# Optimization experiments

Hardware: AMD Instinct MI355X
Metric: run time of the kernel (lower is better)

Reference implementation:

```python
import jax, jax.numpy as jnp
import numpy as np

B, S, H = 8, 1024, 1024
NH, HD = 16, 64
MBANK, TOPK = 128, 16
NLAYERS, FF = 12, 4096
EPS = 1e-5


def _ln(x, w, b):
    m = x.mean(-1, keepdims=True)
    v = ((x - m) ** 2).mean(-1, keepdims=True)
    return (x - m) / jnp.sqrt(v + EPS) * w + b


def _split_heads(x):  # [B,S,H] -> [B,NH,S,HD]
    return x.reshape(B, S, NH, HD).transpose(0, 2, 1, 3)


def _sdpa(q, k, v):  # inputs [B,NH,S,HD]
    scores = jnp.einsum('bhqd,bhkd->bhqk', q, k) / jnp.sqrt(jnp.float32(HD))
    attn = jax.nn.softmax(scores, axis=-1)
    o = jnp.einsum('bhqk,bhkd->bhqd', attn, v)
    return o.transpose(0, 2, 1, 3).reshape(B, S, H)


def setup_inputs() -> dict:
    key = jax.random.key(0)
    ks = jax.random.split(key, 24)
    n = lambda k, shp, s=0.02: jax.random.normal(k, shp, jnp.float32) * s
    return {
        'hidden_states': jax.random.normal(ks[0], (B, S, H), jnp.float32),
        'ln1_w': jnp.ones((H,), jnp.float32), 'ln1_b': jnp.zeros((H,), jnp.float32),
        'ln2_w': jnp.ones((H,), jnp.float32), 'ln2_b': jnp.zeros((H,), jnp.float32),
        'rec_wq': n(ks[1], (H, H)), 'rec_wk': n(ks[2], (H, H)),
        'rec_wv': n(ks[3], (H, H)), 'rec_wo': n(ks[4], (H, H)),
        'rec_ad_w1': n(ks[5], (H // 4, H)), 'rec_ad_w2': n(ks[6], (H, H // 4)),
        'mem_bank': n(ks[7], (MBANK, H)),
        'alloc_w': n(ks[8], (MBANK, H)), 'alloc_b': jnp.zeros((MBANK,), jnp.float32),
        'retr_w': n(ks[9], (MBANK, H)), 'retr_b': jnp.zeros((MBANK,), jnp.float32),
        'upd_w': n(ks[10], (H, H)), 'upd_b': jnp.zeros((H,), jnp.float32),
        'mem_scales': jnp.full((NLAYERS,), 0.1, jnp.float32),
        'attn_in_w': n(ks[11], (3 * H, H)), 'attn_in_b': jnp.zeros((3 * H,), jnp.float32),
        'attn_out_w': n(ks[12], (H, H)), 'attn_out_b': jnp.zeros((H,), jnp.float32),
        'mlp_w1': n(ks[13], (FF, H)), 'mlp_b1': jnp.zeros((FF,), jnp.float32),
        'mlp_w2': n(ks[14], (H, FF)), 'mlp_b2': jnp.zeros((H,), jnp.float32),
        'layer_idx': 4,
    }


def reference(hidden_states, ln1_w, ln1_b, ln2_w, ln2_b,
              rec_wq, rec_wk, rec_wv, rec_wo, rec_ad_w1, rec_ad_w2,
              mem_bank, alloc_w, alloc_b, retr_w, retr_b, upd_w, upd_b, mem_scales,
              attn_in_w, attn_in_b, attn_out_w, attn_out_b,
              mlp_w1, mlp_b1, mlp_w2, mlp_b2, layer_idx):
    residual = hidden_states
    h = _ln(hidden_states, ln1_w, ln1_b)

    # --- CrossLayerParameterRecycler (layer_idx % 4 == 0 and > 0 -> recycle) ---
    if layer_idx % 4 == 0 and layer_idx > 0:
        q = _split_heads(h @ rec_wq.T)
        k = _split_heads(h @ rec_wk.T)
        v = _split_heads(h @ rec_wv.T)
        base_out = _sdpa(q, k, v) @ rec_wo.T
        h = jax.nn.relu(base_out @ rec_ad_w1.T) @ rec_ad_w2.T

    # --- CrossLayerMemoryManager ---
    pooled = h.mean(axis=1)                                  # [B,H]
    alloc_weights = jax.nn.softmax(pooled @ alloc_w.T + alloc_b, axis=-1)   # [B,MBANK]
    retr_weights = jax.nn.softmax(pooled @ retr_w.T + retr_b, axis=-1)
    retrieved = retr_weights @ mem_bank                      # [B,H]
    h = h + retrieved[:, None, :] * mem_scales[layer_idx]
    update_signals = jax.nn.sigmoid(h.mean(axis=1) @ upd_w.T + upd_b)       # [B,H]
    _, top_idx = jax.lax.top_k(alloc_weights, TOPK)          # [B,TOPK]

    # sequential per-batch scatter (later batches overwrite earlier, as in torch loop)
    def _write(mb, be):
        idx, sig = be
        return mb.at[idx].set(jnp.broadcast_to(sig, (TOPK, H))), None
    new_mem_bank, _ = jax.lax.scan(_write, mem_bank, (top_idx, update_signals))

    # --- self attention (nn.MultiheadAttention, batch_first) ---
    qkv = h @ attn_in_w.T + attn_in_b                        # [B,S,3H]
    q, k, v = jnp.split(qkv, 3, axis=-1)
    attn_out = _sdpa(_split_heads(q), _split_heads(k), _split_heads(v))
    attn_out = attn_out @ attn_out_w.T + attn_out_b
    h = residual + attn_out

    # --- MLP block ---
    residual2 = h
    h = _ln(h, ln2_w, ln2_b)
    h = jax.nn.gelu(h @ mlp_w1.T + mlp_b1, approximate=False) @ mlp_w2.T + mlp_b2
    out = residual2 + h
    return out, new_mem_bank
```

## Files before the change

### kernel.cpp

```cpp
#include <hip/hip_runtime.h>
#include <hip/hip_bf16.h>
#include <math.h>
#include <stdint.h>


#define BB 8
#define SS 1024
#define HH 1024
#define NHEAD 16
#define HD 64
#define MBANK 128
#define TOPK_N 16
#define FF_DIM 4096
#define MROWS (BB * SS)
#define NB_ELEM (8ull*1024*1024)

typedef __bf16 bf16x8 __attribute__((ext_vector_type(8)));
typedef __bf16 bf16x4 __attribute__((ext_vector_type(4)));
typedef float f32x4 __attribute__((ext_vector_type(4)));

#define SCALE_LOG2E 0.18033688011112042f

__device__ __forceinline__ unsigned short f2b(float x) {
  unsigned u = __float_as_uint(x);
  unsigned r = (u + 0x7FFFu + ((u >> 16) & 1u)) >> 16;
  return (unsigned short)r;
}
__device__ __forceinline__ float b2f(unsigned short u) {
  return __uint_as_float((unsigned)u << 16);
}

__device__ __forceinline__ float hmax4(f32x4 v) {
  return fmaxf(fmaxf(v[0], v[1]), fmaxf(v[2], v[3]));
}

__device__ __forceinline__ void load16_lds(const void* g, void* lds_base, int lane) {
#if __has_builtin(__builtin_amdgcn_global_load_lds)
  typedef const __attribute__((address_space(1))) unsigned int guint;
  typedef __attribute__((address_space(3))) unsigned int luint;
  __builtin_amdgcn_global_load_lds((guint*)(uintptr_t)g,
                                   (luint*)(unsigned long long)(unsigned int)(uintptr_t)lds_base,
                                   16, 0, 0);
#else
  *(uint4*)((char*)lds_base + lane * 16) = *(const uint4*)g;
#endif
}

__device__ __forceinline__ float gelu_exact(float x) {
  return 0.5f * x * (1.f + erff(x * 0.70710678118654752440f));
}


__global__ __launch_bounds__(256) void cast_split(const float* __restrict__ s,
                                                  unsigned short* __restrict__ hi,
                                                  unsigned short* __restrict__ lo, int n4) {
  int i = blockIdx.x * 256 + threadIdx.x;
  if (i < n4) {
    float4 v = ((const float4*)s)[i];
    ushort4 h, l;
    h.x = f2b(v.x); l.x = f2b(v.x - b2f(h.x));
    h.y = f2b(v.y); l.y = f2b(v.y - b2f(h.y));
    h.z = f2b(v.z); l.z = f2b(v.z - b2f(h.z));
    h.w = f2b(v.w); l.w = f2b(v.w - b2f(h.w));
    ((ushort4*)hi)[i] = h;
    ((ushort4*)lo)[i] = l;
  }
}

__global__ __launch_bounds__(256) void ln3(const float* __restrict__ x,
                                           const float* __restrict__ w,
                                           const float* __restrict__ b,
                                           unsigned short* __restrict__ yh,
                                           unsigned short* __restrict__ yl) {
  int row = blockIdx.x;
  const float* xr = x + (size_t)row * HH;
  int t = threadIdx.x;
  float v[4];
  float s = 0.f, ss = 0.f;
#pragma unroll
  for (int i = 0; i < 4; i++) {
    v[i] = xr[t + i * 256];
    s += v[i];
    ss += v[i] * v[i];
  }
  __shared__ float rs[8], rss[8];
  for (int o = 32; o > 0; o >>= 1) {
    s += __shfl_down(s, o, 64);
    ss += __shfl_down(ss, o, 64);
  }
  int wid = t >> 6, lane = t & 63;
  if (lane == 0) { rs[wid] = s; rss[wid] = ss; }
  __syncthreads();
  if (t == 0) {
    float S = rs[0] + rs[1] + rs[2] + rs[3];
    float SSum = rss[0] + rss[1] + rss[2] + rss[3];
    float m = S * (1.f / HH);
    float var = SSum * (1.f / HH) - m * m;
    rs[4] = m;
    rs[5] = rsqrtf(var + 1e-5f);
  }
  __syncthreads();
  float m = rs[4], inv = rs[5];
#pragma unroll
  for (int i = 0; i < 4; i++) {
    int c = t + i * 256;
    float y = (v[i] - m) * inv * w[c] + b[c];
    unsigned short h = f2b(y);
    yh[(size_t)row * HH + c] = h;
    yl[(size_t)row * HH + c] = f2b(y - b2f(h));
  }
}

template <int ACT, int MODE>
__global__ __launch_bounds__(256) void gemm3(const unsigned short* __restrict__ Ah,
                                             const unsigned short* __restrict__ Al, int lda,
                                             const unsigned short* __restrict__ Wh,
                                             const unsigned short* __restrict__ Wl, int ldw,
                                             unsigned short* __restrict__ Oh,
                                             unsigned short* __restrict__ Ol,
                                             float* __restrict__ outF,
                                             int ldo, int K) {
  __shared__ unsigned short Ash[128 * 32];
  __shared__ unsigned short Asl[128 * 32];
  __shared__ unsigned short Bsh[128 * 32];
  __shared__ unsigned short Bsl[128 * 32];
  int n0 = blockIdx.x * 128, m0 = blockIdx.y * 128;
  int t = threadIdx.x, w = t >> 6, L = t & 63, quad = L >> 4, l16 = L & 15;
  int wm = w & 1, wn = w >> 1;
  const f32x4 vzero = {0.f, 0.f, 0.f, 0.f};
  f32x4 acc[4][4];
#pragma unroll
  for (int i = 0; i < 4; i++)
#pragma unroll
    for (int j = 0; j < 4; j++) acc[i][j] = vzero;
  int srow = L >> 2;
  int scol = ((L & 3) ^ ((L >> 3) & 3)) * 8;
  int rsw = (l16 >> 1) & 3;
  for (int k0 = 0; k0 < K; k0 += 32) {
    __syncthreads();
#pragma unroll
    for (int c = 0; c < 2; c++) {
      int r = (c * 4 + w) * 16 + srow;
      size_t aoff = (size_t)(m0 + r) * lda + k0 + scol;
      size_t boff = (size_t)(n0 + r) * ldw + k0 + scol;
      load16_lds(Ah + aoff, &Ash[(c * 4 + w) * 512], L);
      load16_lds(Al + aoff, &Asl[(c * 4 + w) * 512], L);
      load16_lds(Wh + boff, &Bsh[(c * 4 + w) * 512], L);
      load16_lds(Wl + boff, &Bsl[(c * 4 + w) * 512], L);
    }
    __syncthreads();
    bf16x8 afh[4], afl[4], bfh[4], bfl[4];
#pragma unroll
    for (int i = 0; i < 4; i++) {
      int off = (wm * 64 + i * 16 + l16) * 32 + (quad ^ rsw) * 8;
      afh[i] = *(const bf16x8*)&Ash[off];
      afl[i] = *(const bf16x8*)&Asl[off];
    }
#pragma unroll
    for (int j = 0; j < 4; j++) {
      int off = (wn * 64 + j * 16 + l16) * 32 + (quad ^ rsw) * 8;
      bfh[j] = *(const bf16x8*)&Bsh[off];
      bfl[j] = *(const bf16x8*)&Bsl[off];
    }
#pragma unroll
    for (int i = 0; i < 4; i++)
#pragma unroll
      for (int j = 0; j < 4; j++) {
        acc[i][j] = __builtin_amdgcn_mfma_f32_16x16x32_bf16(afh[i], bfh[j], acc[i][j], 0, 0, 0);
        acc[i][j] = __builtin_amdgcn_mfma_f32_16x16x32_bf16(afh[i], bfl[j], acc[i][j], 0, 0, 0);
        acc[i][j] = __builtin_amdgcn_mfma_f32_16x16x32_bf16(afl[i], bfh[j], acc[i][j], 0, 0, 0);
      }
  }
#pragma unroll
  for (int i = 0; i < 4; i++) {
    int mb = m0 + wm * 64 + i * 16 + quad * 4;
#pragma unroll
    for (int j = 0; j < 4; j++) {
      int n = n0 + wn * 64 + j * 16 + l16;
      if (MODE == 1) {
        ushort4 sh, sl;
        float vv[4];
#pragma unroll
        for (int r = 0; r < 4; r++) {
          float v = acc[i][j][r];
          if (ACT == 1) v = fmaxf(v, 0.f);
          vv[r] = v;
        }
        sh.x = f2b(vv[0]); sl.x = f2b(vv[0] - b2f(sh.x));
        sh.y = f2b(vv[1]); sl.y = f2b(vv[1] - b2f(sh.y));
        sh.z = f2b(vv[2]); sl.z = f2b(vv[2] - b2f(sh.z));
        sh.w = f2b(vv[3]); sl.w = f2b(vv[3] - b2f(sh.w));
        *(ushort4*)&Oh[(size_t)n * ldo + mb] = sh;
        *(ushort4*)&Ol[(size_t)n * ldo + mb] = sl;
      } else {
#pragma unroll
        for (int r = 0; r < 4; r++) {
          float v = acc[i][j][r];
          if (ACT == 1) v = fmaxf(v, 0.f);
          size_t off = (size_t)(mb + r) * ldo + n;
          if (MODE == 0) {
            unsigned short h = f2b(v);
            Oh[off] = h;
            Ol[off] = f2b(v - b2f(h));
          } else {
            outF[off] = v;
          }
        }
      }
    }
  }
}

__global__ __launch_bounds__(256) void sdpa3(const unsigned short* __restrict__ Qh,
                                             const unsigned short* __restrict__ Ql,
                                             const unsigned short* __restrict__ Kh,
                                             const unsigned short* __restrict__ Kl,
                                             const unsigned short* __restrict__ Vth,
                                             const unsigned short* __restrict__ Vtl,
                                             unsigned short* __restrict__ Oh,
                                             unsigned short* __restrict__ Ol) {
  __shared__ unsigned short Ksh[64 * 64];
  __shared__ unsigned short Ksl[64 * 64];
  __shared__ unsigned short Vsh[64 * 64];
  __shared__ unsigned short Vsl[64 * 64];
  __shared__ __align__(16) unsigned short Psh[4][16 * 64];
  __shared__ __align__(16) unsigned short Psl[4][16 * 64];
  int qt = blockIdx.x, h = blockIdx.y, b = blockIdx.z;
  int t = threadIdx.x, w = t >> 6, L = t & 63, quad = L >> 4, l16 = L & 15;
  int q0 = qt * 64;
  const f32x4 vzero = {0.f, 0.f, 0.f, 0.f};
  bf16x8 qfh[2], qfl[2];
  {
    size_t qrow = (size_t)(b * SS + q0 + w * 16 + l16);
#pragma unroll
    for (int kh = 0; kh < 2; kh++) {
      size_t off = qrow * HH + h * 64 + kh * 32 + quad * 8;
      qfh[kh] = *(const bf16x8*)&Qh[off];
      qfl[kh] = *(const bf16x8*)&Ql[off];
    }
  }
  float mprev = -1e30f, lsum = 0.f;
  f32x4 oacc[4];
#pragma unroll
  for (int jd = 0; jd < 4; jd++) oacc[jd] = vzero;
  int srow = L >> 3, scol = ((L & 7) ^ (L >> 3)) * 8;
  int k7 = l16 & 7;
  unsigned short* Pwh = &Psh[w][0];
  unsigned short* Pwl = &Psl[w][0];
  for (int k0 = 0; k0 < SS; k0 += 64) {
    __syncthreads();
#pragma unroll
    for (int c = 0; c < 2; c++) {
      int rr = (c * 4 + w) * 8 + srow;
      size_t koff = (size_t)(b * SS + k0 + rr) * HH + h * 64 + scol;
      size_t voff = (size_t)(h * 64 + rr) * MROWS + b * SS + k0 + scol;
      load16_lds(Kh + koff, &Ksh[(c * 4 + w) * 512], L);
      load16_lds(Kl + koff, &Ksl[(c * 4 + w) * 512], L);
      load16_lds(Vth + voff, &Vsh[(c * 4 + w) * 512], L);
      load16_lds(Vtl + voff, &Vsl[(c * 4 + w) * 512], L);
    }
    __syncthreads();
    f32x4 sacc[4];
#pragma unroll
    for (int jn = 0; jn < 4; jn++) sacc[jn] = vzero;
#pragma unroll
    for (int jn = 0; jn < 4; jn++)
#pragma unroll
      for (int kh = 0; kh < 2; kh++) {
        int off = (jn * 16 + l16) * 64 + ((kh * 4 + quad) ^ k7) * 8;
        bf16x8 kfh = *(const bf16x8*)&Ksh[off];
        bf16x8 kfl = *(const bf16x8*)&Ksl[off];
        sacc[jn] = __builtin_amdgcn_mfma_f32_16x16x32_bf16(kfh, qfh[kh], sacc[jn], 0, 0, 0);
        sacc[jn] = __builtin_amdgcn_mfma_f32_16x16x32_bf16(kfl, qfh[kh], sacc[jn], 0, 0, 0);
        sacc[jn] = __builtin_amdgcn_mfma_f32_16x16x32_bf16(kfh, qfl[kh], sacc[jn], 0, 0, 0);
      }
    float mt = fmaxf(fmaxf(hmax4(sacc[0]), hmax4(sacc[1])),
                     fmaxf(hmax4(sacc[2]), hmax4(sacc[3])));
    mt = fmaxf(mt, __shfl_xor(mt, 16, 64));
    mt = fmaxf(mt, __shfl_xor(mt, 32, 64));
    float m2 = fmaxf(mprev, mt * SCALE_LOG2E);
    float alpha = exp2f(mprev - m2);
    mprev = m2;
    float rs = 0.f;
#pragma unroll
    for (int jn = 0; jn < 4; jn++) {
      float p0 = exp2f(fmaf(sacc[jn][0], SCALE_LOG2E, -m2));
      float p1 = exp2f(fmaf(sacc[jn][1], SCALE_LOG2E, -m2));
      float p2 = exp2f(fmaf(sacc[jn][2], SCALE_LOG2E, -m2));
      float p3 = exp2f(fmaf(sacc[jn][3], SCALE_LOG2E, -m2));
      rs += (p0 + p1) + (p2 + p3);
      bf16x4 ph, pl;
      ph[0] = (__bf16)p0; pl[0] = (__bf16)(p0 - (float)ph[0]);
      ph[1] = (__bf16)p1; pl[1] = (__bf16)(p1 - (float)ph[1]);
      ph[2] = (__bf16)p2; pl[2] = (__bf16)(p2 - (float)ph[2]);
      ph[3] = (__bf16)p3; pl[3] = (__bf16)(p3 - (float)ph[3]);
      int pidx = l16 * 64 + (((jn * 2 + (quad >> 1)) ^ k7) << 3) + ((quad & 1) << 2);
      *(bf16x4*)&Pwh[pidx] = ph;
      *(bf16x4*)&Pwl[pidx] = pl;
    }
    rs += __shfl_xor(rs, 16, 64);
    rs += __shfl_xor(rs, 32, 64);
    lsum = lsum * alpha + rs;
    float ar[4];
#pragma unroll
    for (int r = 0; r < 4; r++) ar[r] = __shfl(alpha, quad * 4 + r, 16);
#pragma unroll
    for (int jd = 0; jd < 4; jd++)
#pragma unroll
      for (int r = 0; r < 4; r++) oacc[jd][r] *= ar[r];
    bf16x8 pfh[2], pfl[2];
#pragma unroll
    for (int kh = 0; kh < 2; kh++) {
      int off = l16 * 64 + (((kh * 4 + quad) ^ k7) << 3);
      pfh[kh] = *(const bf16x8*)&Pwh[off];
      pfl[kh] = *(const bf16x8*)&Pwl[off];
    }
#pragma unroll
    for (int jd = 0; jd < 4; jd++)
#pragma unroll
      for (int kh = 0; kh < 2; kh++) {
        int off = (jd * 16 + l16) * 64 + ((kh * 4 + quad) ^ k7) * 8;
        bf16x8 vfh = *(const bf16x8*)&Vsh[off];
        bf16x8 vfl = *(const bf16x8*)&Vsl[off];
        oacc[jd] = __builtin_amdgcn_mfma_f32_16x16x32_bf16(pfh[kh], vfh, oacc[jd], 0, 0, 0);
        oacc[jd] = __builtin_amdgcn_mfma_f32_16x16x32_bf16(pfh[kh], vfl, oacc[jd], 0, 0, 0);
        oacc[jd] = __builtin_amdgcn_mfma_f32_16x16x32_bf16(pfl[kh], vfh, oacc[jd], 0, 0, 0);
      }
  }
  float inv = 1.f / lsum;
  float invr[4];
#pragma unroll
  for (int r = 0; r < 4; r++) invr[r] = __shfl(inv, quad * 4 + r, 16);
#pragma unroll
  for (int r = 0; r < 4; r++) {
    size_t row = (size_t)(b * SS + q0 + w * 16 + quad * 4 + r);
#pragma unroll
    for (int jd = 0; jd < 4; jd++) {
      float v = oacc[jd][r] * invr[r];
      unsigned short hh = f2b(v);
      size_t off = row * HH + h * 64 + jd * 16 + l16;
      Oh[off] = hh;
      Ol[off] = f2b(v - b2f(hh));
    }
  }
}


__global__ __launch_bounds__(256) void meanpool_kernel(const float* __restrict__ Hb,
                                                       float* __restrict__ P) {
  int cb = blockIdx.x;
  int b = blockIdx.y;
  int t = threadIdx.x;
  int c = (t & 63) + cb * 64;
  int part = t >> 6;
  float s = 0.f;
  const float* p = Hb + ((size_t)b * SS + part * 256) * HH + c;
  for (int j = 0; j < 256; j++) s += p[(size_t)j * HH];
  __shared__ float red[4][64];
  red[part][t & 63] = s;
  __syncthreads();
  if (t < 64) {
    float tot = red[0][t] + red[1][t] + red[2][t] + red[3][t];
    P[b * HH + cb * 64 + t] = tot * (1.f / SS);
  }
}

__global__ __launch_bounds__(256) void memlogits_kernel(const float* __restrict__ P,
                                                        const float* __restrict__ AW,
                                                        const float* __restrict__ ABias,
                                                        const float* __restrict__ RW,
                                                        const float* __restrict__ RBias,
                                                        float* __restrict__ LA,
                                                        float* __restrict__ LR) {
  int m = blockIdx.x, b = blockIdx.y;
  int t = threadIdx.x;
  const float* pr = P + b * HH;
  const float* aw = AW + (size_t)m * HH;
  const float* rw = RW + (size_t)m * HH;
  float sa = 0.f, sr = 0.f;
  for (int i = t; i < HH; i += 256) {
    float pv = pr[i];
    sa = fmaf(pv, aw[i], sa);
    sr = fmaf(pv, rw[i], sr);
  }
  for (int o = 32; o > 0; o >>= 1) {
    sa += __shfl_down(sa, o, 64);
    sr += __shfl_down(sr, o, 64);
  }
  __shared__ float ra[4], rr[4];
  if ((t & 63) == 0) { ra[t >> 6] = sa; rr[t >> 6] = sr; }
  __syncthreads();
  if (t == 0) {
    LA[b * MBANK + m] = ra[0] + ra[1] + ra[2] + ra[3] + ABias[m];
    LR[b * MBANK + m] = rr[0] + rr[1] + rr[2] + rr[3] + RBias[m];
  }
}

__global__ __launch_bounds__(256) void retrieve_kernel(const float* __restrict__ LA,
                                                       const float* __restrict__ LR,
                                                       const float* __restrict__ MB,
                                                       float* __restrict__ RET,
                                                       int* __restrict__ ISTOP) {
  int b = blockIdx.x;
  int t = threadIdx.x;
  __shared__ float rw[MBANK];
  __shared__ float la[MBANK];
  if (t < MBANK) {
    la[t] = LA[b * MBANK + t];
    rw[t] = LR[b * MBANK + t];
  }
  __syncthreads();
  if (t == 0) {
    float mx = -1e30f;
    for (int i = 0; i < MBANK; i++) mx = fmaxf(mx, rw[i]);
    float s = 0.f;
    for (int i = 0; i < MBANK; i++) {
      float e = __expf(rw[i] - mx);
      rw[i] = e;
      s += e;
    }
    float inv = 1.f / s;
    for (int i = 0; i < MBANK; i++) rw[i] *= inv;
  }
  __syncthreads();
  if (t < MBANK) {
    float mine = la[t];
    int rank = 0;
    for (int i = 0; i < MBANK; i++) {
      float o = la[i];
      if (o > mine || (o == mine && i < t)) rank++;
    }
    ISTOP[b * MBANK + t] = (rank < TOPK_N) ? 1 : 0;
  }
  for (int c = t; c < HH; c += 256) {
    float s = 0.f;
    for (int m = 0; m < MBANK; m++) s = fmaf(rw[m], MB[(size_t)m * HH + c], s);
    RET[b * HH + c] = s;
  }
}

__global__ __launch_bounds__(256) void addmem_kernel(float* __restrict__ Hb,
                                                     const float* __restrict__ RET,
                                                     const float* __restrict__ scales,
                                                     const int* __restrict__ lidx) {
  float sc = scales[lidx[0]];
  size_t i = (size_t)blockIdx.x * 256 + threadIdx.x;
  int c = (int)(i & 1023);
  int b = (int)(i >> 20);
  Hb[i] = fmaf(RET[b * HH + c], sc, Hb[i]);
}

__global__ __launch_bounds__(256) void upd_kernel(const float* __restrict__ P2,
                                                  const float* __restrict__ UW,
                                                  const float* __restrict__ UB,
                                                  float* __restrict__ UPD) {
  int n = blockIdx.x, b = blockIdx.y;
  int t = threadIdx.x;
  const float* pr = P2 + b * HH;
  const float* wr = UW + (size_t)n * HH;
  float s = 0.f;
  for (int i = t; i < HH; i += 256) s = fmaf(pr[i], wr[i], s);
  for (int o = 32; o > 0; o >>= 1) s += __shfl_down(s, o, 64);
  __shared__ float red[4];
  if ((t & 63) == 0) red[t >> 6] = s;
  __syncthreads();
  if (t == 0) {
    float tot = red[0] + red[1] + red[2] + red[3] + UB[n];
    UPD[b * HH + n] = 1.f / (1.f + __expf(-tot));
  }
}

__global__ __launch_bounds__(256) void membank_kernel(const float* __restrict__ MB,
                                                      const int* __restrict__ ISTOP,
                                                      const float* __restrict__ UPD,
                                                      float* __restrict__ OUT) {
  int row = blockIdx.x;
  int col = blockIdx.y * 256 + threadIdx.x;
  int w = -1;
  for (int b = 0; b < BB; b++)
    if (ISTOP[b * MBANK + row]) w = b;
  float v = (w >= 0) ? UPD[w * HH + col] : MB[(size_t)row * HH + col];
  OUT[(size_t)row * HH + col] = v;
}


__global__ __launch_bounds__(256) void ln_bf(const float* __restrict__ x,
                                             const float* __restrict__ w,
                                             const float* __restrict__ b,
                                             unsigned short* __restrict__ y) {
  int row = blockIdx.x;
  const float* xr = x + (size_t)row * HH;
  unsigned short* yr = y + (size_t)row * HH;
  int t = threadIdx.x;
  float v[4];
  float s = 0.f, ss = 0.f;
#pragma unroll
  for (int i = 0; i < 4; i++) {
    v[i] = xr[t + i * 256];
    s += v[i];
    ss += v[i] * v[i];
  }
  __shared__ float rs[8], rss[8];
  for (int o = 32; o > 0; o >>= 1) {
    s += __shfl_down(s, o, 64);
    ss += __shfl_down(ss, o, 64);
  }
  int wid = t >> 6, lane = t & 63;
  if (lane == 0) { rs[wid] = s; rss[wid] = ss; }
  __syncthreads();
  if (t == 0) {
    float S = rs[0] + rs[1] + rs[2] + rs[3];
    float SSum = rss[0] + rss[1] + rss[2] + rss[3];
    float m = S * (1.f / HH);
    float var = SSum * (1.f / HH) - m * m;
    rs[4] = m;
    rs[5] = rsqrtf(var + 1e-5f);
  }
  __syncthreads();
  float m = rs[4], inv = rs[5];
#pragma unroll
  for (int i = 0; i < 4; i++) {
    int c = t + i * 256;
    yr[c] = f2b((v[i] - m) * inv * w[c] + b[c]);
  }
}

__global__ __launch_bounds__(256) void castf2b(const float* __restrict__ s,
                                               unsigned short* __restrict__ d, int n4) {
  int i = blockIdx.x * 256 + threadIdx.x;
  if (i < n4) {
    float4 v = ((const float4*)s)[i];
    ushort4 o;
    o.x = f2b(v.x); o.y = f2b(v.y); o.z = f2b(v.z); o.w = f2b(v.w);
    ((ushort4*)d)[i] = o;
  }
}

template <int ACT, int MODE>
__global__ __launch_bounds__(256) void gemm_bf(const unsigned short* __restrict__ A, int lda,
                                               const unsigned short* __restrict__ W, int ldw,
                                               const float* __restrict__ bias,
                                               const float* __restrict__ resid,
                                               float* __restrict__ outF,
                                               unsigned short* __restrict__ outB,
                                               int ldo, int K) {
  __shared__ unsigned short As[128 * 32];
  __shared__ unsigned short Bs[128 * 32];
  int n0 = blockIdx.x * 128, m0 = blockIdx.y * 128;
  int t = threadIdx.x, w = t >> 6, L = t & 63, quad = L >> 4, l16 = L & 15;
  int wm = w & 1, wn = w >> 1;
  const f32x4 vzero = {0.f, 0.f, 0.f, 0.f};
  f32x4 acc[4][4];
#pragma unroll
  for (int i = 0; i < 4; i++)
#pragma unroll
    for (int j = 0; j < 4; j++) acc[i][j] = vzero;
  int srow = L >> 2;
  int scol = ((L & 3) ^ ((L >> 3) & 3)) * 8;
  int rsw = (l16 >> 1) & 3;
  for (int k0 = 0; k0 < K; k0 += 32) {
    __syncthreads();
#pragma unroll
    for (int c = 0; c < 2; c++) {
      int r = (c * 4 + w) * 16 + srow;
      load16_lds(A + (size_t)(m0 + r) * lda + k0 + scol, &As[(c * 4 + w) * 512], L);
      load16_lds(W + (size_t)(n0 + r) * ldw + k0 + scol, &Bs[(c * 4 + w) * 512], L);
    }
    __syncthreads();
    bf16x8 af[4], bfr[4];
#pragma unroll
    for (int i = 0; i < 4; i++)
      af[i] = *(const bf16x8*)&As[(wm * 64 + i * 16 + l16) * 32 + (quad ^ rsw) * 8];
#pragma unroll
    for (int j = 0; j < 4; j++)
      bfr[j] = *(const bf16x8*)&Bs[(wn * 64 + j * 16 + l16) * 32 + (quad ^ rsw) * 8];
#pragma unroll
    for (int i = 0; i < 4; i++)
#pragma unroll
      for (int j = 0; j < 4; j++)
        acc[i][j] = __builtin_amdgcn_mfma_f32_16x16x32_bf16(af[i], bfr[j], acc[i][j], 0, 0, 0);
  }
#pragma unroll
  for (int i = 0; i < 4; i++) {
    int mb = m0 + wm * 64 + i * 16 + quad * 4;
#pragma unroll
    for (int j = 0; j < 4; j++) {
      int n = n0 + wn * 64 + j * 16 + l16;
      float bv = bias ? bias[n] : 0.f;
      if (MODE == 2) {
        ushort4 st;
        float v0 = acc[i][j][0] + bv, v1 = acc[i][j][1] + bv;
        float v2 = acc[i][j][2] + bv, v3 = acc[i][j][3] + bv;
        if (ACT == 1) { v0 = fmaxf(v0, 0.f); v1 = fmaxf(v1, 0.f); v2 = fmaxf(v2, 0.f); v3 = fmaxf(v3, 0.f); }
        if (ACT == 2) { v0 = gelu_exact(v0); v1 = gelu_exact(v1); v2 = gelu_exact(v2); v3 = gelu_exact(v3); }
        st.x = f2b(v0); st.y = f2b(v1); st.z = f2b(v2); st.w = f2b(v3);
        *(ushort4*)&outB[(size_t)n * ldo + mb] = st;
      } else {
#pragma unroll
        for (int r = 0; r < 4; r++) {
          float v = acc[i][j][r] + bv;
          if (ACT == 1) v = fmaxf(v, 0.f);
          if (ACT == 2) v = gelu_exact(v);
          size_t off = (size_t)(mb + r) * ldo + n;
          if (MODE == 1) outB[off] = f2b(v);
          else if (MODE == 3) outF[off] += v;
          else if (MODE == 4) outF[off] = v + resid[off];
        }
      }
    }
  }
}

__global__ __launch_bounds__(256) void sdpa_bf(const unsigned short* __restrict__ Q,
                                               const unsigned short* __restrict__ Kb,
                                               const unsigned short* __restrict__ Vt,
                                               unsigned short* __restrict__ O) {
  __shared__ unsigned short Ks[64 * 64];
  __shared__ unsigned short Vs[64 * 64];
  __shared__ __align__(16) unsigned short Ps[4][16 * 64];
  int qt = blockIdx.x, h = blockIdx.y, b = blockIdx.z;
  int t = threadIdx.x, w = t >> 6, L = t & 63, quad = L >> 4, l16 = L & 15;
  int q0 = qt * 64;
  const f32x4 vzero = {0.f, 0.f, 0.f, 0.f};
  bf16x8 qf[2];
  {
    size_t qrow = (size_t)(b * SS + q0 + w * 16 + l16);
#pragma unroll
    for (int kh = 0; kh < 2; kh++)
      qf[kh] = *(const bf16x8*)&Q[qrow * HH + h * 64 + kh * 32 + quad * 8];
  }
  float mprev = -1e30f, lsum = 0.f;
  f32x4 oacc[4];
#pragma unroll
  for (int jd = 0; jd < 4; jd++) oacc[jd] = vzero;
  int srow = L >> 3, scol = ((L & 7) ^ (L >> 3)) * 8;
  int k7 = l16 & 7;
  unsigned short* Pw = &Ps[w][0];
  for (int k0 = 0; k0 < SS; k0 += 64) {
    __syncthreads();
#pragma unroll
    for (int c = 0; c < 2; c++) {
      int rr = (c * 4 + w) * 8 + srow;
      load16_lds(Kb + (size_t)(b * SS + k0 + rr) * HH + h * 64 + scol, &Ks[(c * 4 + w) * 512], L);
      load16_lds(Vt + (size_t)(h * 64 + rr) * MROWS + b * SS + k0 + scol, &Vs[(c * 4 + w) * 512], L);
    }
    __syncthreads();
    f32x4 sacc[4];
#pragma unroll
    for (int jn = 0; jn < 4; jn++) sacc[jn] = vzero;
#pragma unroll
    for (int jn = 0; jn < 4; jn++)
#pragma unroll
      for (int kh = 0; kh < 2; kh++) {
        bf16x8 kf = *(const bf16x8*)&Ks[(jn * 16 + l16) * 64 + ((kh * 4 + quad) ^ k7) * 8];
        sacc[jn] = __builtin_amdgcn_mfma_f32_16x16x32_bf16(kf, qf[kh], sacc[jn], 0, 0, 0);
      }
    float mt = fmaxf(fmaxf(hmax4(sacc[0]), hmax4(sacc[1])),
                     fmaxf(hmax4(sacc[2]), hmax4(sacc[3])));
    mt = fmaxf(mt, __shfl_xor(mt, 16, 64));
    mt = fmaxf(mt, __shfl_xor(mt, 32, 64));
    float m2 = fmaxf(mprev, mt * SCALE_LOG2E);
    float alpha = exp2f(mprev - m2);
    mprev = m2;
    float rs = 0.f;
#pragma unroll
    for (int jn = 0; jn < 4; jn++) {
      float p0 = exp2f(fmaf(sacc[jn][0], SCALE_LOG2E, -m2));
      float p1 = exp2f(fmaf(sacc[jn][1], SCALE_LOG2E, -m2));
      float p2 = exp2f(fmaf(sacc[jn][2], SCALE_LOG2E, -m2));
      float p3 = exp2f(fmaf(sacc[jn][3], SCALE_LOG2E, -m2));
      rs += (p0 + p1) + (p2 + p3);
      bf16x4 pk;
      pk[0] = (__bf16)p0; pk[1] = (__bf16)p1; pk[2] = (__bf16)p2; pk[3] = (__bf16)p3;
      *(bf16x4*)&Pw[l16 * 64 + (((jn * 2 + (quad >> 1)) ^ k7) << 3) + ((quad & 1) << 2)] = pk;
    }
    rs += __shfl_xor(rs, 16, 64);
    rs += __shfl_xor(rs, 32, 64);
    lsum = lsum * alpha + rs;
    float ar[4];
#pragma unroll
    for (int r = 0; r < 4; r++) ar[r] = __shfl(alpha, quad * 4 + r, 16);
#pragma unroll
    for (int jd = 0; jd < 4; jd++)
#pragma unroll
      for (int r = 0; r < 4; r++) oacc[jd][r] *= ar[r];
    bf16x8 pf[2];
#pragma unroll
    for (int kh = 0; kh < 2; kh++)
      pf[kh] = *(const bf16x8*)&Pw[l16 * 64 + (((kh * 4 + quad) ^ k7) << 3)];
#pragma unroll
    for (int jd = 0; jd < 4; jd++)
#pragma unroll
      for (int kh = 0; kh < 2; kh++) {
        bf16x8 vf = *(const bf16x8*)&Vs[(jd * 16 + l16) * 64 + ((kh * 4 + quad) ^ k7) * 8];
        oacc[jd] = __builtin_amdgcn_mfma_f32_16x16x32_bf16(pf[kh], vf, oacc[jd], 0, 0, 0);
      }
  }
  float inv = 1.f / lsum;
  float invr[4];
#pragma unroll
  for (int r = 0; r < 4; r++) invr[r] = __shfl(inv, quad * 4 + r, 16);
#pragma unroll
  for (int r = 0; r < 4; r++) {
    size_t row = (size_t)(b * SS + q0 + w * 16 + quad * 4 + r);
#pragma unroll
    for (int jd = 0; jd < 4; jd++)
      O[row * HH + h * 64 + jd * 16 + l16] = f2b(oacc[jd][r] * invr[r]);
  }
}

extern "C" void kernel_launch(void* const* d_in, const int* in_sizes, int n_in,
                              void* d_out, int out_size, void* d_ws, size_t ws_size,
                              hipStream_t stream) {
  const float* x = (const float*)d_in[0];
  const float* ln1_w = (const float*)d_in[1];
  const float* ln1_b = (const float*)d_in[2];
  const float* ln2_w = (const float*)d_in[3];
  const float* ln2_b = (const float*)d_in[4];
  const float* rec_wq = (const float*)d_in[5];
  const float* rec_wk = (const float*)d_in[6];
  const float* rec_wv = (const float*)d_in[7];
  const float* rec_wo = (const float*)d_in[8];
  const float* rec_ad_w1 = (const float*)d_in[9];
  const float* rec_ad_w2 = (const float*)d_in[10];
  const float* mem_bank = (const float*)d_in[11];
  const float* alloc_w = (const float*)d_in[12];
  const float* alloc_b = (const float*)d_in[13];
  const float* retr_w = (const float*)d_in[14];
  const float* retr_b = (const float*)d_in[15];
  const float* upd_w = (const float*)d_in[16];
  const float* upd_b = (const float*)d_in[17];
  const float* mem_scales = (const float*)d_in[18];
  const float* attn_in_w = (const float*)d_in[19];
  const float* attn_in_b = (const float*)d_in[20];
  const float* attn_out_w = (const float*)d_in[21];
  const float* attn_out_b = (const float*)d_in[22];
  const float* mlp_w1 = (const float*)d_in[23];
  const float* mlp_b1 = (const float*)d_in[24];
  const float* mlp_w2 = (const float*)d_in[25];
  const float* mlp_b2 = (const float*)d_in[26];
  const int* layer_idx = (const int*)d_in[27];

  float* out = (float*)d_out;
  float* out_mb = out + NB_ELEM;

  const size_t U = NB_ELEM;
  unsigned short* W16 = (unsigned short*)d_ws;
  unsigned short* U0 = W16;
  unsigned short* U1 = W16 + U;
  unsigned short* U2 = W16 + 2 * U;
  unsigned short* U3 = W16 + 3 * U;
  unsigned short* U4 = W16 + 4 * U;
  unsigned short* U5 = W16 + 5 * U;
  unsigned short* wsh = W16 + 6 * U;
  unsigned short* wsl = wsh + 1048576;
  float* small = (float*)(wsl + 1048576);
  float* pooled = small;
  float* pooled2 = small + 8192;
  float* logitsA = small + 16384;
  float* logitsR = small + 17408;
  float* retrieved = small + 18432;
  float* updsig = small + 26624;
  int* istop = (int*)(small + 34816);
  unsigned short* D0 = (unsigned short*)out;
  unsigned short* D1 = D0 + U;
  unsigned short* ain_bf = U5;
  unsigned short* aout_bf = U5 + 3 * 1048576;

  dim3 blk(256);
  dim3 gG(8, 64);
  dim3 gG256(2, 64);
  dim3 gS(16, NHEAD, BB);
  const int EW_GRID = (int)(NB_ELEM / 256);

  ln3<<<MROWS, blk, 0, stream>>>(x, ln1_w, ln1_b, U0, U1);
  cast_split<<<1024, blk, 0, stream>>>(rec_wq, wsh, wsl, 262144);
  gemm3<0, 0><<<gG, blk, 0, stream>>>(U0, U1, HH, wsh, wsl, HH, U2, U3, nullptr, HH, HH);
  cast_split<<<1024, blk, 0, stream>>>(rec_wk, wsh, wsl, 262144);
  gemm3<0, 0><<<gG, blk, 0, stream>>>(U0, U1, HH, wsh, wsl, HH, U4, U5, nullptr, HH, HH);
  cast_split<<<1024, blk, 0, stream>>>(rec_wv, wsh, wsl, 262144);
  gemm3<0, 1><<<gG, blk, 0, stream>>>(U0, U1, HH, wsh, wsl, HH, D0, D1, nullptr, MROWS, HH);
  sdpa3<<<gS, blk, 0, stream>>>(U2, U3, U4, U5, D0, D1, U0, U1);
  cast_split<<<1024, blk, 0, stream>>>(rec_wo, wsh, wsl, 262144);
  gemm3<0, 0><<<gG, blk, 0, stream>>>(U0, U1, HH, wsh, wsl, HH, U2, U3, nullptr, HH, HH);
  cast_split<<<256, blk, 0, stream>>>(rec_ad_w1, wsh, wsl, 65536);
  gemm3<1, 0><<<gG256, blk, 0, stream>>>(U2, U3, HH, wsh, wsl, HH, U4, U4 + 2097152, nullptr, 256, HH);
  cast_split<<<256, blk, 0, stream>>>(rec_ad_w2, wsh, wsl, 65536);
  gemm3<0, 2><<<gG, blk, 0, stream>>>(U4, U4 + 2097152, 256, wsh, wsl, 256, nullptr, nullptr, out, HH, 256);
  meanpool_kernel<<<dim3(HH / 64, BB), blk, 0, stream>>>(out, pooled);
  memlogits_kernel<<<dim3(MBANK, BB), blk, 0, stream>>>(pooled, alloc_w, alloc_b, retr_w, retr_b, logitsA, logitsR);
  retrieve_kernel<<<BB, blk, 0, stream>>>(logitsA, logitsR, mem_bank, retrieved, istop);
  addmem_kernel<<<EW_GRID, blk, 0, stream>>>(out, retrieved, mem_scales, layer_idx);
  meanpool_kernel<<<dim3(HH / 64, BB), blk, 0, stream>>>(out, pooled2);
  upd_kernel<<<dim3(HH, BB), blk, 0, stream>>>(pooled2, upd_w, upd_b, updsig);
  membank_kernel<<<dim3(MBANK, HH / 256), blk, 0, stream>>>(mem_bank, istop, updsig, out_mb);
  castf2b<<<8192, blk, 0, stream>>>(out, U0, 2097152);
  castf2b<<<3072, blk, 0, stream>>>(attn_in_w, ain_bf, 786432);
  castf2b<<<1024, blk, 0, stream>>>(attn_out_w, aout_bf, 262144);
  gemm_bf<0, 1><<<gG, blk, 0, stream>>>(U0, HH, ain_bf, HH, attn_in_b, nullptr, nullptr, U1, HH, HH);
  gemm_bf<0, 1><<<gG, blk, 0, stream>>>(U0, HH, ain_bf + (size_t)HH * HH, HH, attn_in_b + HH, nullptr, nullptr, U2, HH, HH);
  gemm_bf<0, 2><<<gG, blk, 0, stream>>>(U0, HH, ain_bf + 2ull * HH * HH, HH, attn_in_b + 2 * HH, nullptr, nullptr, U3, MROWS, HH);
  sdpa_bf<<<gS, blk, 0, stream>>>(U1, U2, U3, U4);
  gemm_bf<0, 4><<<gG, blk, 0, stream>>>(U4, HH, aout_bf, HH, attn_out_b, x, out, nullptr, HH, HH);
  ln_bf<<<MROWS, blk, 0, stream>>>(out, ln2_w, ln2_b, U1);
  {
    unsigned short* w1b = U0;
    unsigned short* w2b = U0 + 4 * 1048576;
    unsigned short* h2 = U2;
    castf2b<<<4096, blk, 0, stream>>>(mlp_w1, w1b, 1048576);
    castf2b<<<4096, blk, 0, stream>>>(mlp_w2, w2b, 1048576);
    gemm_bf<2, 1><<<dim3(32, 64), blk, 0, stream>>>(U1, HH, w1b, HH, mlp_b1, nullptr, nullptr, h2, FF_DIM, HH);
    gemm_bf<0, 3><<<gG, blk, 0, stream>>>(h2, FF_DIM, w2b, FF_DIM, mlp_b2, nullptr, out, nullptr, HH, FF_DIM);
  }
}
```

Baseline: 1.282 ms.

## Keep softmax probabilities in registers by permuting K rows in attention kernels

Both attention kernels (split-precision sdpa3 and bf16 sdpa_bf) now permute which K rows each lane loads, so the S accumulator's per-lane layout directly matches the A-operand layout needed for the P·V MFMA. This removes the per-wave LDS scratch buffer for P and its store/load round trip each key tile. K's LDS swizzle is changed to match the new row mapping, which risks bank conflicts or a wrong permutation if the index maths is off.

Result: faster. 1.254 ms (-2.2%).

```diff
diff --git a/kernel.cpp b/kernel.cpp
--- a/kernel.cpp
+++ b/kernel.cpp
@@ -223,8 +223,6 @@
   __shared__ unsigned short Ksl[64 * 64];
   __shared__ unsigned short Vsh[64 * 64];
   __shared__ unsigned short Vsl[64 * 64];
-  __shared__ __align__(16) unsigned short Psh[4][16 * 64];
-  __shared__ __align__(16) unsigned short Psl[4][16 * 64];
   int qt = blockIdx.x, h = blockIdx.y, b = blockIdx.z;
   int t = threadIdx.x, w = t >> 6, L = t & 63, quad = L >> 4, l16 = L & 15;
   int q0 = qt * 64;
@@ -243,17 +241,19 @@
   f32x4 oacc[4];
 #pragma unroll
   for (int jd = 0; jd < 4; jd++) oacc[jd] = vzero;
-  int srow = L >> 3, scol = ((L & 7) ^ (L >> 3)) * 8;
+  int srow = L >> 3;
+  int scolV = ((L & 7) ^ srow) * 8;
+  int rbase = ((l16 & 12) << 1) | (l16 & 3);
+  int keyK = (l16 & 3) | (((l16 >> 2) & 1) << 2);
   int k7 = l16 & 7;
-  unsigned short* Pwh = &Psh[w][0];
-  unsigned short* Pwl = &Psl[w][0];
   for (int k0 = 0; k0 < SS; k0 += 64) {
     __syncthreads();
 #pragma unroll
     for (int c = 0; c < 2; c++) {
       int rr = (c * 4 + w) * 8 + srow;
-      size_t koff = (size_t)(b * SS + k0 + rr) * HH + h * 64 + scol;
-      size_t voff = (size_t)(h * 64 + rr) * MROWS + b * SS + k0 + scol;
+      int scolK = ((L & 7) ^ ((srow & 3) | (((c * 4 + w) & 1) << 2))) * 8;
+      size_t koff = (size_t)(b * SS + k0 + rr) * HH + h * 64 + scolK;
+      size_t voff = (size_t)(h * 64 + rr) * MROWS + b * SS + k0 + scolV;
       load16_lds(Kh + koff, &Ksh[(c * 4 + w) * 512], L);
       load16_lds(Kl + koff, &Ksl[(c * 4 + w) * 512], L);
       load16_lds(Vth + voff, &Vsh[(c * 4 + w) * 512], L);
@@ -264,16 +264,18 @@
 #pragma unroll
     for (int jn = 0; jn < 4; jn++) sacc[jn] = vzero;
 #pragma unroll
-    for (int jn = 0; jn < 4; jn++)
+    for (int jn = 0; jn < 4; jn++) {
+      int rowp = rbase + (jn & 1) * 4 + (jn >> 1) * 32;
 #pragma unroll
       for (int kh = 0; kh < 2; kh++) {
-        int off = (jn * 16 + l16) * 64 + ((kh * 4 + quad) ^ k7) * 8;
+        int off = rowp * 64 + (((kh * 4 + quad) ^ keyK) << 3);
         bf16x8 kfh = *(const bf16x8*)&Ksh[off];
         bf16x8 kfl = *(const bf16x8*)&Ksl[off];
         sacc[jn] = __builtin_amdgcn_mfma_f32_16x16x32_bf16(kfh, qfh[kh], sacc[jn], 0, 0, 0);
         sacc[jn] = __builtin_amdgcn_mfma_f32_16x16x32_bf16(kfl, qfh[kh], sacc[jn], 0, 0, 0);
         sacc[jn] = __builtin_amdgcn_mfma_f32_16x16x32_bf16(kfh, qfl[kh], sacc[jn], 0, 0, 0);
       }
+    }
     float mt = fmaxf(fmaxf(hmax4(sacc[0]), hmax4(sacc[1])),
                      fmaxf(hmax4(sacc[2]), hmax4(sacc[3])));
     mt = fmaxf(mt, __shfl_xor(mt, 16, 64));
@@ -282,21 +284,18 @@
     float alpha = exp2f(mprev - m2);
     mprev = m2;
     float rs = 0.f;
+    bf16x8 pah[2], pal[2];
 #pragma unroll
     for (int jn = 0; jn < 4; jn++) {
-      float p0 = exp2f(fmaf(sacc[jn][0], SCALE_LOG2E, -m2));
-      float p1 = exp2f(fmaf(sacc[jn][1], SCALE_LOG2E, -m2));
-      float p2 = exp2f(fmaf(sacc[jn][2], SCALE_LOG2E, -m2));
-      float p3 = exp2f(fmaf(sacc[jn][3], SCALE_LOG2E, -m2));
-      rs += (p0 + p1) + (p2 + p3);
-      bf16x4 ph, pl;
-      ph[0] = (__bf16)p0; pl[0] = (__bf16)(p0 - (float)ph[0]);
-      ph[1] = (__bf16)p1; pl[1] = (__bf16)(p1 - (float)ph[1]);
-      ph[2] = (__bf16)p2; pl[2] = (__bf16)(p2 - (float)ph[2]);
-      ph[3] = (__bf16)p3; pl[3] = (__bf16)(p3 - (float)ph[3]);
-      int pidx = l16 * 64 + (((jn * 2 + (quad >> 1)) ^ k7) << 3) + ((quad & 1) << 2);
-      *(bf16x4*)&Pwh[pidx] = ph;
-      *(bf16x4*)&Pwl[pidx] = pl;
+      int kh = jn >> 1, half = (jn & 1) * 4;
+#pragma unroll
+      for (int r = 0; r < 4; r++) {
+        float p = exp2f(fmaf(sacc[jn][r], SCALE_LOG2E, -m2));
+        rs += p;
+        __bf16 ph = (__bf16)p;
+        pah[kh][half + r] = ph;
+        pal[kh][half + r] = (__bf16)(p - (float)ph);
+      }
     }
     rs += __shfl_xor(rs, 16, 64);
     rs += __shfl_xor(rs, 32, 64);
@@ -308,13 +307,6 @@
     for (int jd = 0; jd < 4; jd++)
 #pragma unroll
       for (int r = 0; r < 4; r++) oacc[jd][r] *= ar[r];
-    bf16x8 pfh[2], pfl[2];
-#pragma unroll
-    for (int kh = 0; kh < 2; kh++) {
-      int off = l16 * 64 + (((kh * 4 + quad) ^ k7) << 3);
-      pfh[kh] = *(const bf16x8*)&Pwh[off];
-      pfl[kh] = *(const bf16x8*)&Pwl[off];
-    }
 #pragma unroll
     for (int jd = 0; jd < 4; jd++)
 #pragma unroll
@@ -322,9 +314,9 @@
         int off = (jd * 16 + l16) * 64 + ((kh * 4 + quad) ^ k7) * 8;
         bf16x8 vfh = *(const bf16x8*)&Vsh[off];
         bf16x8 vfl = *(const bf16x8*)&Vsl[off];
-        oacc[jd] = __builtin_amdgcn_mfma_f32_16x16x32_bf16(pfh[kh], vfh, oacc[jd], 0, 0, 0);
-        oacc[jd] = __builtin_amdgcn_mfma_f32_16x16x32_bf16(pfh[kh], vfl, oacc[jd], 0, 0, 0);
-        oacc[jd] = __builtin_amdgcn_mfma_f32_16x16x32_bf16(pfl[kh], vfh, oacc[jd], 0, 0, 0);
+        oacc[jd] = __builtin_amdgcn_mfma_f32_16x16x32_bf16(pah[kh], vfh, oacc[jd], 0, 0, 0);
+        oacc[jd] = __builtin_amdgcn_mfma_f32_16x16x32_bf16(pah[kh], vfl, oacc[jd], 0, 0, 0);
+        oacc[jd] = __builtin_amdgcn_mfma_f32_16x16x32_bf16(pal[kh], vfh, oacc[jd], 0, 0, 0);
       }
   }
   float inv = 1.f / lsum;
@@ -617,7 +609,6 @@
                                                unsigned short* __restrict__ O) {
   __shared__ unsigned short Ks[64 * 64];
   __shared__ unsigned short Vs[64 * 64];
-  __shared__ __align__(16) unsigned short Ps[4][16 * 64];
   int qt = blockIdx.x, h = blockIdx.y, b = blockIdx.z;
   int t = threadIdx.x, w = t >> 6, L = t & 63, quad = L >> 4, l16 = L & 15;
   int q0 = qt * 64;
@@ -633,28 +624,33 @@
   f32x4 oacc[4];
 #pragma unroll
   for (int jd = 0; jd < 4; jd++) oacc[jd] = vzero;
-  int srow = L >> 3, scol = ((L & 7) ^ (L >> 3)) * 8;
+  int srow = L >> 3;
+  int scolV = ((L & 7) ^ srow) * 8;
+  int rbase = ((l16 & 12) << 1) | (l16 & 3);
+  int keyK = (l16 & 3) | (((l16 >> 2) & 1) << 2);
   int k7 = l16 & 7;
-  unsigned short* Pw = &Ps[w][0];
   for (int k0 = 0; k0 < SS; k0 += 64) {
     __syncthreads();
 #pragma unroll
     for (int c = 0; c < 2; c++) {
       int rr = (c * 4 + w) * 8 + srow;
-      load16_lds(Kb + (size_t)(b * SS + k0 + rr) * HH + h * 64 + scol, &Ks[(c * 4 + w) * 512], L);
-      load16_lds(Vt + (size_t)(h * 64 + rr) * MROWS + b * SS + k0 + scol, &Vs[(c * 4 + w) * 512], L);
+      int scolK = ((L & 7) ^ ((srow & 3) | (((c * 4 + w) & 1) << 2))) * 8;
+      load16_lds(Kb + (size_t)(b * SS + k0 + rr) * HH + h * 64 + scolK, &Ks[(c * 4 + w) * 512], L);
+      load16_lds(Vt + (size_t)(h * 64 + rr) * MROWS + b * SS + k0 + scolV, &Vs[(c * 4 + w) * 512], L);
     }
     __syncthreads();
     f32x4 sacc[4];
 #pragma unroll
     for (int jn = 0; jn < 4; jn++) sacc[jn] = vzero;
 #pragma unroll
-    for (int jn = 0; jn < 4; jn++)
+    for (int jn = 0; jn < 4; jn++) {
+      int rowp = rbase + (jn & 1) * 4 + (jn >> 1) * 32;
 #pragma unroll
       for (int kh = 0; kh < 2; kh++) {
-        bf16x8 kf = *(const bf16x8*)&Ks[(jn * 16 + l16) * 64 + ((kh * 4 + quad) ^ k7) * 8];
+        bf16x8 kf = *(const bf16x8*)&Ks[rowp * 64 + (((kh * 4 + quad) ^ keyK) << 3)];
         sacc[jn] = __builtin_amdgcn_mfma_f32_16x16x32_bf16(kf, qf[kh], sacc[jn], 0, 0, 0);
       }
+    }
     float mt = fmaxf(fmaxf(hmax4(sacc[0]), hmax4(sacc[1])),
                      fmaxf(hmax4(sacc[2]), hmax4(sacc[3])));
     mt = fmaxf(mt, __shfl_xor(mt, 16, 64));
@@ -663,16 +659,16 @@
     float alpha = exp2f(mprev - m2);
     mprev = m2;
     float rs = 0.f;
+    bf16x8 pa[2];
 #pragma unroll
     for (int jn = 0; jn < 4; jn++) {
-      float p0 = exp2f(fmaf(sacc[jn][0], SCALE_LOG2E, -m2));
-      float p1 = exp2f(fmaf(sacc[jn][1], SCALE_LOG2E, -m2));
-      float p2 = exp2f(fmaf(sacc[jn][2], SCALE_LOG2E, -m2));
-      float p3 = exp2f(fmaf(sacc[jn][3], SCALE_LOG2E, -m2));
-      rs += (p0 + p1) + (p2 + p3);
-      bf16x4 pk;
-      pk[0] = (__bf16)p0; pk[1] = (__bf16)p1; pk[2] = (__bf16)p2; pk[3] = (__bf16)p3;
-      *(bf16x4*)&Pw[l16 * 64 + (((jn * 2 + (quad >> 1)) ^ k7) << 3) + ((quad & 1) << 2)] = pk;
+      int kh = jn >> 1, half = (jn & 1) * 4;
+#pragma unroll
+      for (int r = 0; r < 4; r++) {
+        float p = exp2f(fmaf(sacc[jn][r], SCALE_LOG2E, -m2));
+        rs += p;
+        pa[kh][half + r] = (__bf16)p;
+      }
     }
     rs += __shfl_xor(rs, 16, 64);
     rs += __shfl_xor(rs, 32, 64);
@@ -684,16 +680,12 @@
     for (int jd = 0; jd < 4; jd++)
 #pragma unroll
       for (int r = 0; r < 4; r++) oacc[jd][r] *= ar[r];
-    bf16x8 pf[2];
-#pragma unroll
-    for (int kh = 0; kh < 2; kh++)
-      pf[kh] = *(const bf16x8*)&Pw[l16 * 64 + (((kh * 4 + quad) ^ k7) << 3)];
 #pragma unroll
     for (int jd = 0; jd < 4; jd++)
 #pragma unroll
       for (int kh = 0; kh < 2; kh++) {
         bf16x8 vf = *(const bf16x8*)&Vs[(jd * 16 + l16) * 64 + ((kh * 4 + quad) ^ k7) * 8];
-        oacc[jd] = __builtin_amdgcn_mfma_f32_16x16x32_bf16(pf[kh], vf, oacc[jd], 0, 0, 0);
+        oacc[jd] = __builtin_amdgcn_mfma_f32_16x16x32_bf16(pa[kh], vf, oacc[jd], 0, 0, 0);
       }
   }
   float inv = 1.f / lsum;
```
